# Kernel optimization log

Measured on AMD Instinct MI355X. Metric: run time of the kernel, lower is better.

## Reference

```python
import jax, jax.numpy as jnp
import numpy as np

D_MODEL, HIDDEN, H, NB = 1024, 128, 16, 32
B, L = 4, 4096


def setup_inputs() -> dict:
    key = jax.random.key(0)
    ks = jax.random.split(key, 6)
    theta_path = jax.random.normal(ks[0], (B, L, H, NB), dtype=jnp.float32)
    content_emb = jax.random.normal(ks[1], (B, L, D_MODEL), dtype=jnp.float32)
    # params (log_Pi init 0.0; final linear weight scaled by 0.01, bias 0, as in torch init)
    log_Pi = jnp.zeros((H, NB), dtype=jnp.float32)
    W1 = jax.random.normal(ks[2], (D_MODEL, HIDDEN), dtype=jnp.float32) / np.sqrt(D_MODEL)
    b1 = jnp.zeros((HIDDEN,), dtype=jnp.float32)
    W2 = (jax.random.normal(ks[3], (HIDDEN, H * NB), dtype=jnp.float32) / np.sqrt(HIDDEN)) * 0.01
    b2 = jnp.zeros((H * NB,), dtype=jnp.float32)
    return {"theta_path": theta_path, "content_emb": content_emb,
            "log_Pi": log_Pi, "W1": W1, "b1": b1, "W2": W2, "b2": b2}


def _affine_combine(c1, c2):
    a1, u1 = c1
    a2, u2 = c2
    return a2 * a1, a2 * u1 + u2


def reference(theta_path, content_emb, log_Pi, W1, b1, W2, b2):
    Bx, Lx, Hx, NBx = theta_path.shape
    # log_R_head: Linear -> GELU(exact) -> Linear, then clamp
    h = jax.nn.gelu(content_emb @ W1 + b1, approximate=False)
    log_R = jnp.clip((h @ W2 + b2).reshape(Bx, Lx, Hx, NBx), -5.0, 5.0)
    R = jnp.exp(log_R)
    # wrapped innovation nu = atan2(sin(-theta), cos(-theta))
    nu = jnp.arctan2(jnp.sin(-theta_path), jnp.cos(-theta_path))
    Pi = jnp.exp(log_Pi)[None, None]            # [1,1,H,NB]
    K = Pi / jnp.maximum(Pi + R, 1e-8)
    alpha = 1.0 - K
    u = K * nu
    # affine recurrence d_t = alpha_t * d_{t-1} + u_t, parallel scan over L
    _, d = jax.lax.associative_scan(_affine_combine, (alpha, u), axis=1)
    return theta_path + d, jnp.broadcast_to(Pi, R.shape), K, R
```

## Files before the change

### kernel.cpp

```cpp
#include <hip/hip_runtime.h>
#include <math.h>

#define B_   4
#define L_   4096
#define H_   16
#define NB_  32
#define C_   512
#define DM_  1024
#define HID_ 128
#define M_   (B_*L_)
#define NC_  128
#define CT_  32

typedef __attribute__((ext_vector_type(8))) short short8;
typedef __attribute__((ext_vector_type(4))) float f32x4;

__device__ __forceinline__ unsigned short f2bf(float f) {
  unsigned u = __float_as_uint(f);
  u += 0x7fffu + ((u >> 16) & 1u);
  return (unsigned short)(u >> 16);
}

__device__ __forceinline__ float wrap_neg(float th) {
  return 6.283185307179586f * rintf(th * 0.15915494309189535f) - th;
}

__global__ __launch_bounds__(256) void k_prep(const float* __restrict__ W1,
                                              const float* __restrict__ W2,
                                              unsigned short* __restrict__ W1T,
                                              unsigned short* __restrict__ W2T) {
  int idx = blockIdx.x * 256 + threadIdx.x;
  if (idx < DM_ * HID_) {
    int n = idx >> 10, k = idx & 1023;
    W1T[idx] = f2bf(W1[(size_t)k * HID_ + n]);
  }
  int i2 = idx - DM_ * HID_;
  if (i2 >= 0 && i2 < HID_ * C_) {
    int n = i2 >> 7, k = i2 & 127;
    W2T[i2] = f2bf(W2[(size_t)k * C_ + n]);
  }
}

__global__ __launch_bounds__(512) void k_gemm1(const float* __restrict__ X,
                                               const unsigned short* __restrict__ W1T,
                                               const float* __restrict__ b1,
                                               unsigned short* __restrict__ Hb) {
  __shared__ char lds[24576];
  const int tid  = threadIdx.x;
  const int m0   = blockIdx.x * 64;
  const int lane = tid & 63;
  const int wave = tid >> 6;
  const int wr   = wave >> 2;
  const int wc   = wave & 3;
  const int fr   = lane & 15;
  const int kg   = lane >> 4;

  f32x4 acc[2][2];
#pragma unroll
  for (int i = 0; i < 2; ++i)
#pragma unroll
    for (int j = 0; j < 2; ++j) acc[i][j] = (f32x4){0.f, 0.f, 0.f, 0.f};

  for (int k0 = 0; k0 < DM_; k0 += 64) {
    {
      int row = tid >> 3, k8 = tid & 7;
      const float4* src = (const float4*)(X + (size_t)(m0 + row) * DM_ + k0 + k8 * 8);
      float4 v0 = src[0], v1 = src[1];
      uint4 pk;
      pk.x = f2bf(v0.x) | ((unsigned)f2bf(v0.y) << 16);
      pk.y = f2bf(v0.z) | ((unsigned)f2bf(v0.w) << 16);
      pk.z = f2bf(v1.x) | ((unsigned)f2bf(v1.y) << 16);
      pk.w = f2bf(v1.z) | ((unsigned)f2bf(v1.w) << 16);
      *(uint4*)(lds + row * 128 + ((k8 ^ (row & 7)) << 4)) = pk;
    }
#pragma unroll
    for (int t = 0; t < 2; ++t) {
      int c = tid + t * 512;
      int n = c >> 3, k8 = c & 7;
      uint4 v = *(const uint4*)(W1T + (size_t)n * DM_ + k0 + k8 * 8);
      *(uint4*)(lds + 8192 + n * 128 + ((k8 ^ (n & 7)) << 4)) = v;
    }
    __syncthreads();
#pragma unroll
    for (int ks = 0; ks < 2; ++ks) {
      short8 a[2], b[2];
#pragma unroll
      for (int i = 0; i < 2; ++i) {
        int row = wr * 32 + i * 16 + fr;
        a[i] = *(const short8*)(lds + row * 128 + (((ks * 4 + kg) ^ (row & 7)) << 4));
      }
#pragma unroll
      for (int j = 0; j < 2; ++j) {
        int col = wc * 32 + j * 16 + fr;
        b[j] = *(const short8*)(lds + 8192 + col * 128 + (((ks * 4 + kg) ^ (col & 7)) << 4));
      }
#pragma unroll
      for (int i = 0; i < 2; ++i)
#pragma unroll
        for (int j = 0; j < 2; ++j)
          acc[i][j] = __builtin_amdgcn_mfma_f32_16x16x32_bf16(a[i], b[j], acc[i][j], 0, 0, 0);
    }
    __syncthreads();
  }
#pragma unroll
  for (int i = 0; i < 2; ++i)
#pragma unroll
    for (int j = 0; j < 2; ++j) {
      int col = wc * 32 + j * 16 + fr;
      float bb = b1[col];
#pragma unroll
      for (int r = 0; r < 4; ++r) {
        int row = m0 + wr * 32 + i * 16 + kg * 4 + r;
        float x = acc[i][j][r] + bb;
        float g = 0.5f * x * (1.0f + erff(x * 0.70710678f));
        Hb[(size_t)row * HID_ + col] = f2bf(g);
      }
    }
}

__global__ __launch_bounds__(512) void k_gemm2(const unsigned short* __restrict__ Hb,
                                               const unsigned short* __restrict__ W2T,
                                               const float* __restrict__ b2,
                                               const float* __restrict__ logPi,
                                               float* __restrict__ out1,
                                               float* __restrict__ out2,
                                               float* __restrict__ out3) {
  __shared__ char lds[24576];
  const int tid  = threadIdx.x;
  const int m0   = blockIdx.x * 64;
  const int n0   = blockIdx.y * 128;
  const int lane = tid & 63;
  const int wave = tid >> 6;
  const int wr   = wave >> 2;
  const int wc   = wave & 3;
  const int fr   = lane & 15;
  const int kg   = lane >> 4;

  f32x4 acc[2][2];
#pragma unroll
  for (int i = 0; i < 2; ++i)
#pragma unroll
    for (int j = 0; j < 2; ++j) acc[i][j] = (f32x4){0.f, 0.f, 0.f, 0.f};

  for (int k0 = 0; k0 < HID_; k0 += 64) {
    {
      int row = tid >> 3, k8 = tid & 7;
      uint4 v = *(const uint4*)(Hb + (size_t)(m0 + row) * HID_ + k0 + k8 * 8);
      *(uint4*)(lds + row * 128 + ((k8 ^ (row & 7)) << 4)) = v;
    }
#pragma unroll
    for (int t = 0; t < 2; ++t) {
      int c = tid + t * 512;
      int n = c >> 3, k8 = c & 7;
      uint4 v = *(const uint4*)(W2T + (size_t)(n0 + n) * HID_ + k0 + k8 * 8);
      *(uint4*)(lds + 8192 + n * 128 + ((k8 ^ (n & 7)) << 4)) = v;
    }
    __syncthreads();
#pragma unroll
    for (int ks = 0; ks < 2; ++ks) {
      short8 a[2], b[2];
#pragma unroll
      for (int i = 0; i < 2; ++i) {
        int row = wr * 32 + i * 16 + fr;
        a[i] = *(const short8*)(lds + row * 128 + (((ks * 4 + kg) ^ (row & 7)) << 4));
      }
#pragma unroll
      for (int j = 0; j < 2; ++j) {
        int col = wc * 32 + j * 16 + fr;
        b[j] = *(const short8*)(lds + 8192 + col * 128 + (((ks * 4 + kg) ^ (col & 7)) << 4));
      }
#pragma unroll
      for (int i = 0; i < 2; ++i)
#pragma unroll
        for (int j = 0; j < 2; ++j)
          acc[i][j] = __builtin_amdgcn_mfma_f32_16x16x32_bf16(a[i], b[j], acc[i][j], 0, 0, 0);
    }
    __syncthreads();
  }
#pragma unroll
  for (int i = 0; i < 2; ++i)
#pragma unroll
    for (int j = 0; j < 2; ++j) {
      int col = n0 + wc * 32 + j * 16 + fr;
      float Pi = expf(logPi[col]);
      float bb = b2[col];
#pragma unroll
      for (int r = 0; r < 4; ++r) {
        int row = m0 + wr * 32 + i * 16 + kg * 4 + r;
        float lr = acc[i][j][r] + bb;
        lr = fminf(5.0f, fmaxf(-5.0f, lr));
        float R = expf(lr);
        float K = Pi / fmaxf(Pi + R, 1e-8f);
        size_t o = (size_t)row * C_ + col;
        out1[o] = Pi; out2[o] = K; out3[o] = R;
      }
    }
}

__global__ __launch_bounds__(256) void k_scan1(const float* __restrict__ Kv,
                                               const float* __restrict__ theta,
                                               float* __restrict__ Ab,
                                               float* __restrict__ Ub) {
  const int b  = blockIdx.x / NC_;
  const int ch = blockIdx.x % NC_;
  const int c  = blockIdx.y * 256 + threadIdx.x;
  size_t base = ((size_t)b * L_ + (size_t)ch * CT_) * C_ + c;
  float A = 1.f, U = 0.f;
  for (int j = 0; j < CT_; ++j) {
    size_t idx = base + (size_t)j * C_;
    float k  = Kv[idx];
    float nu = wrap_neg(theta[idx]);
    float a  = 1.f - k;
    U = a * U + k * nu;
    A *= a;
  }
  size_t o = ((size_t)b * NC_ + ch) * C_ + c;
  Ab[o] = A; Ub[o] = U;
}

__global__ __launch_bounds__(256) void k_scan2(const float* __restrict__ Ab,
                                               const float* __restrict__ Ub,
                                               float* __restrict__ D0) {
  const int id = blockIdx.x * 256 + threadIdx.x;
  const int b = id / C_;
  const int c = id % C_;
  float Up = 0.f;
  for (int i = 0; i < NC_; ++i) {
    size_t o = ((size_t)b * NC_ + i) * C_ + c;
    D0[o] = Up;
    Up = Ab[o] * Up + Ub[o];
  }
}

__global__ __launch_bounds__(256) void k_scan3(const float* __restrict__ Kv,
                                               const float* __restrict__ theta,
                                               const float* __restrict__ D0,
                                               float* __restrict__ out0) {
  const int b  = blockIdx.x / NC_;
  const int ch = blockIdx.x % NC_;
  const int c  = blockIdx.y * 256 + threadIdx.x;
  size_t base = ((size_t)b * L_ + (size_t)ch * CT_) * C_ + c;
  float d = D0[((size_t)b * NC_ + ch) * C_ + c];
  for (int j = 0; j < CT_; ++j) {
    size_t idx = base + (size_t)j * C_;
    float k  = Kv[idx];
    float th = theta[idx];
    float nu = wrap_neg(th);
    d = (1.f - k) * d + k * nu;
    out0[idx] = th + d;
  }
}

extern "C" void kernel_launch(void* const* d_in, const int* in_sizes, int n_in,
                              void* d_out, int out_size, void* d_ws, size_t ws_size,
                              hipStream_t stream) {
  const float* theta = (const float*)d_in[0];
  const float* X     = (const float*)d_in[1];
  const float* logPi = (const float*)d_in[2];
  const float* W1    = (const float*)d_in[3];
  const float* b1    = (const float*)d_in[4];
  const float* W2    = (const float*)d_in[5];
  const float* b2    = (const float*)d_in[6];

  float* out = (float*)d_out;
  const size_t S = (size_t)M_ * C_;
  float* out0 = out;
  float* out1 = out + S;
  float* out2 = out + 2 * S;
  float* out3 = out + 3 * S;

  unsigned short* Hb  = (unsigned short*)d_ws;
  unsigned short* W1T = Hb + (size_t)M_ * HID_;
  unsigned short* W2T = W1T + (size_t)DM_ * HID_;
  float* Ab = (float*)(W2T + (size_t)HID_ * C_);
  float* Ub = Ab + (size_t)B_ * NC_ * C_;
  float* D0 = Ub + (size_t)B_ * NC_ * C_;

  hipLaunchKernelGGL(k_prep, dim3(768), dim3(256), 0, stream, W1, W2, W1T, W2T);
  hipLaunchKernelGGL(k_gemm1, dim3(M_ / 64), dim3(512), 0, stream, X, W1T, b1, Hb);
  hipLaunchKernelGGL(k_gemm2, dim3(M_ / 64, C_ / 128), dim3(512), 0, stream,
                     Hb, W2T, b2, logPi, out1, out2, out3);
  hipLaunchKernelGGL(k_scan1, dim3(B_ * NC_, 2), dim3(256), 0, stream, out2, theta, Ab, Ub);
  hipLaunchKernelGGL(k_scan2, dim3(B_ * C_ / 256), dim3(256), 0, stream, Ab, Ub, D0);
  hipLaunchKernelGGL(k_scan3, dim3(B_ * NC_, 2), dim3(256), 0, stream, out2, theta, D0, out0);
}
```

Measured before the change: 85.89 us.

## Fuse chunk scan reduction into GEMM2 epilogue and parallelize carry scan

The first pass of the chunked affine scan moves into the GEMM2 epilogue. Alpha and u go into LDS, and each 64-row tile reduces them to two 32-row chunk summaries, so the separate k_scan1 pass that re-read K and theta is gone. The carry-propagation kernel now splits the 128 chunks into 16 segments with a small LDS scan, replacing 2048 serial threads with more parallel work. Nontemporal loads and stores are added for streaming inputs and outputs. In exchange the GEMM2 block uses about 70KB of LDS, which may cut occupancy, and it now also reads theta in its epilogue.

```diff
diff --git a/kernel.cpp b/kernel.cpp
--- a/kernel.cpp
+++ b/kernel.cpp
@@ -3,8 +3,6 @@
 
 #define B_   4
 #define L_   4096
-#define H_   16
-#define NB_  32
 #define C_   512
 #define DM_  1024
 #define HID_ 128
@@ -64,13 +62,14 @@
   for (int k0 = 0; k0 < DM_; k0 += 64) {
     {
       int row = tid >> 3, k8 = tid & 7;
-      const float4* src = (const float4*)(X + (size_t)(m0 + row) * DM_ + k0 + k8 * 8);
-      float4 v0 = src[0], v1 = src[1];
+      const f32x4* src = (const f32x4*)(X + (size_t)(m0 + row) * DM_ + k0 + k8 * 8);
+      f32x4 v0 = __builtin_nontemporal_load(src);
+      f32x4 v1 = __builtin_nontemporal_load(src + 1);
       uint4 pk;
-      pk.x = f2bf(v0.x) | ((unsigned)f2bf(v0.y) << 16);
-      pk.y = f2bf(v0.z) | ((unsigned)f2bf(v0.w) << 16);
-      pk.z = f2bf(v1.x) | ((unsigned)f2bf(v1.y) << 16);
-      pk.w = f2bf(v1.z) | ((unsigned)f2bf(v1.w) << 16);
+      pk.x = f2bf(v0[0]) | ((unsigned)f2bf(v0[1]) << 16);
+      pk.y = f2bf(v0[2]) | ((unsigned)f2bf(v0[3]) << 16);
+      pk.z = f2bf(v1[0]) | ((unsigned)f2bf(v1[1]) << 16);
+      pk.w = f2bf(v1[2]) | ((unsigned)f2bf(v1[3]) << 16);
       *(uint4*)(lds + row * 128 + ((k8 ^ (row & 7)) << 4)) = pk;
     }
 #pragma unroll
@@ -122,10 +121,17 @@
                                                const unsigned short* __restrict__ W2T,
                                                const float* __restrict__ b2,
                                                const float* __restrict__ logPi,
+                                               const float* __restrict__ theta,
                                                float* __restrict__ out1,
                                                float* __restrict__ out2,
-                                               float* __restrict__ out3) {
-  __shared__ char lds[24576];
+                                               float* __restrict__ out3,
+                                               float* __restrict__ Ab,
+                                               float* __restrict__ Ub) {
+  __shared__ char lds[71808];
+  float* sA  = (float*)lds;
+  float* sU  = sA + 64 * 132;
+  float* sGA = sU + 64 * 132;
+  float* sGU = sGA + 4 * 132;
   const int tid  = threadIdx.x;
   const int m0   = blockIdx.x * 64;
   const int n0   = blockIdx.y * 128;
@@ -177,58 +183,91 @@
     }
     __syncthreads();
   }
+
 #pragma unroll
   for (int i = 0; i < 2; ++i)
 #pragma unroll
     for (int j = 0; j < 2; ++j) {
-      int col = n0 + wc * 32 + j * 16 + fr;
+      int col_l = wc * 32 + j * 16 + fr;
+      int col = n0 + col_l;
       float Pi = expf(logPi[col]);
       float bb = b2[col];
 #pragma unroll
       for (int r = 0; r < 4; ++r) {
-        int row = m0 + wr * 32 + i * 16 + kg * 4 + r;
+        int row_l = wr * 32 + i * 16 + kg * 4 + r;
+        int row = m0 + row_l;
         float lr = acc[i][j][r] + bb;
         lr = fminf(5.0f, fmaxf(-5.0f, lr));
         float R = expf(lr);
         float K = Pi / fmaxf(Pi + R, 1e-8f);
         size_t o = (size_t)row * C_ + col;
-        out1[o] = Pi; out2[o] = K; out3[o] = R;
-      }
-    }
-}
-
-__global__ __launch_bounds__(256) void k_scan1(const float* __restrict__ Kv,
-                                               const float* __restrict__ theta,
-                                               float* __restrict__ Ab,
-                                               float* __restrict__ Ub) {
-  const int b  = blockIdx.x / NC_;
-  const int ch = blockIdx.x % NC_;
-  const int c  = blockIdx.y * 256 + threadIdx.x;
-  size_t base = ((size_t)b * L_ + (size_t)ch * CT_) * C_ + c;
-  float A = 1.f, U = 0.f;
-  for (int j = 0; j < CT_; ++j) {
-    size_t idx = base + (size_t)j * C_;
-    float k  = Kv[idx];
-    float nu = wrap_neg(theta[idx]);
-    float a  = 1.f - k;
-    U = a * U + k * nu;
-    A *= a;
-  }
-  size_t o = ((size_t)b * NC_ + ch) * C_ + c;
-  Ab[o] = A; Ub[o] = U;
+        __builtin_nontemporal_store(Pi, &out1[o]);
+        out2[o] = K;
+        __builtin_nontemporal_store(R, &out3[o]);
+        float nu = wrap_neg(theta[o]);
+        sA[row_l * 132 + col_l] = 1.f - K;
+        sU[row_l * 132 + col_l] = K * nu;
+      }
+    }
+  __syncthreads();
+
+  {
+    int c_l = tid & 127, seg = tid >> 7;
+    float A = 1.f, U = 0.f;
+#pragma unroll
+    for (int rr = seg * 16; rr < seg * 16 + 16; ++rr) {
+      float a = sA[rr * 132 + c_l], u = sU[rr * 132 + c_l];
+      U = a * U + u; A *= a;
+    }
+    sGA[seg * 132 + c_l] = A; sGU[seg * 132 + c_l] = U;
+  }
+  __syncthreads();
+
+  if (tid < 256) {
+    int c_l = tid & 127, h = tid >> 7;
+    float A0 = sGA[(2 * h) * 132 + c_l], U0 = sGU[(2 * h) * 132 + c_l];
+    float A1 = sGA[(2 * h + 1) * 132 + c_l], U1 = sGU[(2 * h + 1) * 132 + c_l];
+    float A = A1 * A0, U = A1 * U0 + U1;
+    int b  = m0 >> 12;
+    int ch = ((m0 & 4095) >> 5) + h;
+    size_t o = ((size_t)(b * NC_ + ch)) * C_ + n0 + c_l;
+    Ab[o] = A; Ub[o] = U;
+  }
 }
 
 __global__ __launch_bounds__(256) void k_scan2(const float* __restrict__ Ab,
                                                const float* __restrict__ Ub,
                                                float* __restrict__ D0) {
-  const int id = blockIdx.x * 256 + threadIdx.x;
-  const int b = id / C_;
-  const int c = id % C_;
-  float Up = 0.f;
-  for (int i = 0; i < NC_; ++i) {
-    size_t o = ((size_t)b * NC_ + i) * C_ + c;
-    D0[o] = Up;
-    Up = Ab[o] * Up + Ub[o];
+  __shared__ float cA[16][17], cU[16][17], carry[16][17];
+  const int tid = threadIdx.x;
+  const int b   = blockIdx.x >> 5;
+  const int c0  = (blockIdx.x & 31) * 16;
+  const int c_l = tid & 15, s = tid >> 4;
+  const int c   = c0 + c_l;
+  float A = 1.f, U = 0.f;
+#pragma unroll
+  for (int k = 0; k < 8; ++k) {
+    size_t o = ((size_t)(b * NC_ + s * 8 + k)) * C_ + c;
+    float a = Ab[o], u = Ub[o];
+    U = a * U + u; A *= a;
+  }
+  cA[s][c_l] = A; cU[s][c_l] = U;
+  __syncthreads();
+  if (tid < 16) {
+    float P = 0.f;
+#pragma unroll
+    for (int ss = 0; ss < 16; ++ss) {
+      carry[ss][tid] = P;
+      P = cA[ss][tid] * P + cU[ss][tid];
+    }
+  }
+  __syncthreads();
+  float d = carry[s][c_l];
+#pragma unroll
+  for (int k = 0; k < 8; ++k) {
+    size_t o = ((size_t)(b * NC_ + s * 8 + k)) * C_ + c;
+    D0[o] = d;
+    d = Ab[o] * d + Ub[o];
   }
 }
 
@@ -240,14 +279,15 @@
   const int ch = blockIdx.x % NC_;
   const int c  = blockIdx.y * 256 + threadIdx.x;
   size_t base = ((size_t)b * L_ + (size_t)ch * CT_) * C_ + c;
-  float d = D0[((size_t)b * NC_ + ch) * C_ + c];
+  float d = D0[((size_t)(b * NC_ + ch)) * C_ + c];
+#pragma unroll 4
   for (int j = 0; j < CT_; ++j) {
     size_t idx = base + (size_t)j * C_;
     float k  = Kv[idx];
     float th = theta[idx];
     float nu = wrap_neg(th);
     d = (1.f - k) * d + k * nu;
-    out0[idx] = th + d;
+    __builtin_nontemporal_store(th + d, &out0[idx]);
   }
 }
 
@@ -279,8 +319,7 @@
   hipLaunchKernelGGL(k_prep, dim3(768), dim3(256), 0, stream, W1, W2, W1T, W2T);
   hipLaunchKernelGGL(k_gemm1, dim3(M_ / 64), dim3(512), 0, stream, X, W1T, b1, Hb);
   hipLaunchKernelGGL(k_gemm2, dim3(M_ / 64, C_ / 128), dim3(512), 0, stream,
-                     Hb, W2T, b2, logPi, out1, out2, out3);
-  hipLaunchKernelGGL(k_scan1, dim3(B_ * NC_, 2), dim3(256), 0, stream, out2, theta, Ab, Ub);
-  hipLaunchKernelGGL(k_scan2, dim3(B_ * C_ / 256), dim3(256), 0, stream, Ab, Ub, D0);
+                     Hb, W2T, b2, logPi, theta, out1, out2, out3, Ab, Ub);
+  hipLaunchKernelGGL(k_scan2, dim3(B_ * 32), dim3(256), 0, stream, Ab, Ub, D0);
   hipLaunchKernelGGL(k_scan3, dim3(B_ * NC_, 2), dim3(256), 0, stream, out2, theta, D0, out0);
 }
```

Result: no change. 85.61 us (-0.3%).
